# Kernel tuning notes

Hardware: AMD Instinct MI355X
Metric: run time of the kernel (lower is better)

## Reference

```python
import jax, jax.numpy as jnp
import numpy as np
from jax import lax

B, T, U, V = 4, 200, 100, 1024
D_ENC, D_DEC, J = 144, 320, 320


def setup_inputs() -> dict:
    key = jax.random.key(0)
    ks = jax.random.split(key, 8)
    s = lambda d: 1.0 / np.sqrt(d).astype(np.float32)
    return {
        "enc_out": jax.random.normal(ks[0], (B, T, D_ENC), jnp.float32),
        "dec_out": jax.random.normal(ks[1], (B, U + 1, D_DEC), jnp.float32),
        "W_enc": jax.random.normal(ks[2], (D_ENC, J), jnp.float32) * s(D_ENC),
        "b_enc": jnp.zeros((J,), jnp.float32),
        "W_dec": jax.random.normal(ks[3], (D_DEC, J), jnp.float32) * s(D_DEC),
        "b_dec": jnp.zeros((J,), jnp.float32),
        "W_out": jax.random.normal(ks[4], (J, V), jnp.float32) * s(J),
        "b_out": jnp.zeros((V,), jnp.float32),
        "targets": jax.random.randint(ks[5], (B, U), 1, V, jnp.int32),
        "enc_lengths": jax.random.randint(ks[6], (B,), T // 2, T + 1, jnp.int32),
        "target_lengths": jax.random.randint(ks[7], (B,), U // 2, U + 1, jnp.int32),
    }


def _rnnt_loss(log_probs, targets, enc_lengths, target_lengths):
    # log_probs: [B, T, U+1, V]; blank index = 0 (matches RNNTLoss(blank=0))
    blank_lp = log_probs[..., 0]  # [B, T, U+1]
    idx = jnp.broadcast_to(targets[:, None, :, None].astype(jnp.int32), (B, T, U, 1))
    emit_lp = jnp.take_along_axis(log_probs[:, :, :U, :], idx, axis=-1)[..., 0]  # [B, T, U]

    # alpha[0, u] = sum of emit log-probs along u at t=0
    alpha0 = jnp.concatenate(
        [jnp.zeros((B, 1), log_probs.dtype), jnp.cumsum(emit_lp[:, 0, :], axis=1)], axis=1
    )  # [B, U+1]

    def row(a, emit_t):
        # a: alpha_prev + blank (vertical transitions), [B, U+1]; emit_t: [B, U]
        def step(prev, xs):
            a_u, e_prev = xs
            cur = jnp.logaddexp(a_u, prev + e_prev)
            return cur, cur
        _, rest = lax.scan(step, a[:, 0], (a[:, 1:].T, emit_t.T))  # rest: [U, B]
        return jnp.concatenate([a[:, :1], rest.T], axis=1)

    def t_step(alpha_prev, xs):
        blank_prev, emit_t = xs
        alpha_t = row(alpha_prev + blank_prev, emit_t)
        return alpha_t, alpha_t

    xs = (jnp.swapaxes(blank_lp[:, :-1, :], 0, 1), jnp.swapaxes(emit_lp[:, 1:, :], 0, 1))
    _, alphas_rest = lax.scan(t_step, alpha0, xs)  # [T-1, B, U+1]
    alphas = jnp.concatenate([alpha0[None], alphas_rest], axis=0)  # [T, B, U+1]

    b_idx = jnp.arange(B)
    t_idx = enc_lengths - 1
    ll = alphas[t_idx, b_idx, target_lengths] + blank_lp[b_idx, t_idx, target_lengths]
    return jnp.mean(-ll)  # reduction='mean' over batch


def reference(enc_out, dec_out, W_enc, b_enc, W_dec, b_dec, W_out, b_out, targets, enc_lengths, target_lengths):
    enc_p = enc_out @ W_enc + b_enc  # [B, T, J]
    dec_p = dec_out @ W_dec + b_dec  # [B, U+1, J]
    joint = jnp.tanh(enc_p[:, :, None, :] + dec_p[:, None, :, :])  # [B, T, U+1, J]
    logits = joint @ W_out + b_out  # [B, T, U+1, V]
    log_probs = jax.nn.log_softmax(logits, axis=-1)
    return _rnnt_loss(log_probs, targets, enc_lengths, target_lengths)
```

## Files before the change

kernel.cpp:

```cpp
#include <hip/hip_runtime.h>
#include <math.h>

#define B_ 4
#define T_ 200
#define U_ 100
#define V_ 1024
#define DE 144
#define DD 320
#define J_ 320
#define M_TOT (B_ * T_ * (U_ + 1))
#define SSTR 328
#define DSTR 104
#define NDIAG 300

typedef __attribute__((ext_vector_type(8))) short bf16x8_t;
typedef __attribute__((ext_vector_type(4))) float f32x4_t;

__device__ __forceinline__ float fast_tanh(float x) {
    float e = __expf(2.0f * x);
    return 1.0f - __fdividef(2.0f, e + 1.0f);
}

__device__ __forceinline__ ushort f2bf(float x) {
    uint u = __float_as_uint(x);
    uint r = (u + 0x7FFFu + ((u >> 16) & 1u)) >> 16;
    return (ushort)r;
}

template <int K>
__global__ __launch_bounds__(J_) void proj_kernel(const float* __restrict__ X,
                                                  const float* __restrict__ W,
                                                  const float* __restrict__ bias,
                                                  float* __restrict__ Y) {
    __shared__ float sx[K];
    const int r = blockIdx.x;
    const int c = threadIdx.x;
    for (int k = threadIdx.x; k < K; k += J_) sx[k] = X[r * K + k];
    __syncthreads();
    float acc = bias[c];
#pragma unroll 4
    for (int k = 0; k < K; k++) acc = fmaf(sx[k], W[k * J_ + c], acc);
    Y[r * J_ + c] = acc;
}

__global__ __launch_bounds__(256) void wconv_kernel(const float* __restrict__ W,
                                                    ushort* __restrict__ Wt) {
    int idx = blockIdx.x * 256 + threadIdx.x;
    int k = idx >> 10;
    int v = idx & 1023;
    ushort b = f2bf(W[idx]);
    int frag = (v >> 4) * 10 + (k >> 5);
    int lane = (v & 15) | (((k >> 3) & 3) << 4);
    int elem = k & 7;
    Wt[frag * 512 + lane * 8 + elem] = b;
}

__global__ __launch_bounds__(1024, 4) void joint_mfma(
    const float* __restrict__ enc_p, const float* __restrict__ dec_p,
    const ushort* __restrict__ Wt, const float* __restrict__ b_out,
    const int* __restrict__ targets,
    float* __restrict__ bsk, float* __restrict__ esk) {
    __shared__ ushort sh[64 * SSTR];
    __shared__ float partm[16][64];
    __shared__ float parts[16][64];
    __shared__ float lse_sh[64];
    __shared__ int tgt_sh[64];

    const int tid = threadIdx.x;
    const int r0 = blockIdx.x * 64;

    for (int q = tid; q < 64 * 80; q += 1024) {
        int i = q / 80;
        int kq = q - i * 80;
        int k0 = kq * 4;
        int rc = r0 + i;
        if (rc > M_TOT - 1) rc = M_TOT - 1;
        int b = rc / 20200;
        int rem = rc - b * 20200;
        int t = rem / 101;
        int u = rem - t * 101;
        float4 e = *(const float4*)&enc_p[(b * 200 + t) * 320 + k0];
        float4 dd = *(const float4*)&dec_p[(b * 101 + u) * 320 + k0];
        ushort4 pk;
        pk.x = f2bf(fast_tanh(e.x + dd.x));
        pk.y = f2bf(fast_tanh(e.y + dd.y));
        pk.z = f2bf(fast_tanh(e.z + dd.z));
        pk.w = f2bf(fast_tanh(e.w + dd.w));
        *(ushort4*)&sh[i * SSTR + k0] = pk;
    }
    if (tid < 64) {
        int rc = r0 + tid;
        int tg = -1;
        if (rc < M_TOT) {
            int b = rc / 20200;
            int rem = rc - b * 20200;
            int u = rem - (rem / 101) * 101;
            if (u < U_) tg = targets[b * U_ + u];
        }
        tgt_sh[tid] = tg;
    }
    __syncthreads();

    const int wave = tid >> 6;
    const int lane = tid & 63;
    const int lrow = lane & 15;
    const int lk = (lane >> 4) * 8;
    const int cb16 = wave * 4;

    f32x4_t acc[4][4];
#pragma unroll
    for (int mt = 0; mt < 4; mt++)
#pragma unroll
        for (int nt = 0; nt < 4; nt++) acc[mt][nt] = (f32x4_t)(0.0f);

    for (int ks = 0; ks < 10; ks++) {
        bf16x8_t a[4];
#pragma unroll
        for (int mt = 0; mt < 4; mt++)
            a[mt] = *(const bf16x8_t*)&sh[(mt * 16 + lrow) * SSTR + ks * 32 + lk];
#pragma unroll
        for (int nt = 0; nt < 4; nt++) {
            bf16x8_t bfr = *(const bf16x8_t*)&Wt[(((cb16 + nt) * 10 + ks) << 9) + lane * 8];
#pragma unroll
            for (int mt = 0; mt < 4; mt++)
                acc[mt][nt] = __builtin_amdgcn_mfma_f32_16x16x32_bf16(a[mt], bfr, acc[mt][nt], 0, 0, 0);
        }
    }

    float bo[4];
#pragma unroll
    for (int nt = 0; nt < 4; nt++) bo[nt] = b_out[wave * 64 + nt * 16 + lrow];
#pragma unroll
    for (int mt = 0; mt < 4; mt++)
#pragma unroll
        for (int nt = 0; nt < 4; nt++) {
            acc[mt][nt].x += bo[nt];
            acc[mt][nt].y += bo[nt];
            acc[mt][nt].z += bo[nt];
            acc[mt][nt].w += bo[nt];
        }

#pragma unroll
    for (int mt = 0; mt < 4; mt++) {
#pragma unroll
        for (int j = 0; j < 4; j++) {
            float m = acc[mt][0][j];
#pragma unroll
            for (int nt = 1; nt < 4; nt++) m = fmaxf(m, acc[mt][nt][j]);
            float s = 0.0f;
#pragma unroll
            for (int nt = 0; nt < 4; nt++) s += __expf(acc[mt][nt][j] - m);
#pragma unroll
            for (int off = 1; off < 16; off <<= 1) {
                float mo = __shfl_xor(m, off, 16);
                float so = __shfl_xor(s, off, 16);
                float M = fmaxf(m, mo);
                s = s * __expf(m - M) + so * __expf(mo - M);
                m = M;
            }
            if (lrow == 0) {
                int row = mt * 16 + (lane >> 4) * 4 + j;
                partm[wave][row] = m;
                parts[wave][row] = s;
            }
        }
    }
    __syncthreads();
    if (tid < 64) {
        float m = partm[0][tid];
        float s = parts[0][tid];
#pragma unroll
        for (int w = 1; w < 16; w++) {
            float mo = partm[w][tid], so = parts[w][tid];
            float M = fmaxf(m, mo);
            s = s * __expf(m - M) + so * __expf(mo - M);
            m = M;
        }
        lse_sh[tid] = m + __logf(s);
    }
    __syncthreads();

#pragma unroll
    for (int mt = 0; mt < 4; mt++) {
#pragma unroll
        for (int j = 0; j < 4; j++) {
            int lr = mt * 16 + (lane >> 4) * 4 + j;
            int r = r0 + lr;
            if (r >= M_TOT) continue;
            int tc = tgt_sh[lr];
            bool isblank = (wave == 0) && (lrow == 0);
            bool isemit = (tc >= 0) && ((tc >> 6) == wave) && ((tc & 15) == lrow);
            if (isblank || isemit) {
                int b = r / 20200;
                int rem = r - b * 20200;
                int t = rem / 101;
                int u = rem - t * 101;
                float lse = lse_sh[lr];
                if (isblank)
                    bsk[(b * NDIAG + t + u) * DSTR + u] = acc[mt][0][j] - lse;
                if (isemit) {
                    int ntl = (tc >> 4) & 3;
                    float v = acc[mt][0][j];
#pragma unroll
                    for (int nt = 1; nt < 4; nt++)
                        if (nt == ntl) v = acc[mt][nt][j];
                    esk[(b * NDIAG + t + u) * DSTR + u] = v - lse;
                }
            }
        }
    }
}

__global__ __launch_bounds__(256) void alpha3_kernel(
    const float* __restrict__ bsk, const float* __restrict__ esk,
    const int* __restrict__ enc_len, const int* __restrict__ tgt_len,
    float* __restrict__ out) {
    __shared__ float ll_sh[B_];
    const int tid = threadIdx.x;
    const int b = tid >> 6;
    const int l = tid & 63;
    const float* Bp = bsk + b * (NDIAG * DSTR);
    const float* Ep = esk + b * (NDIAG * DSTR);
    const int el = enc_len[b];
    const int tl = tgt_len[b];
    const int dfin = el - 1 + tl;

    float a1 = (l == 0) ? 0.0f : -INFINITY;
    float a2 = -INFINITY;

    float c_b1 = Bp[l], c_b2 = Bp[64 + l];
    float c_e1 = Ep[l], c_e2 = Ep[64 + l];
    float m_b1 = Bp[DSTR + l], m_b2 = Bp[DSTR + 64 + l];
    float m_e1 = Ep[DSTR + l], m_e2 = Ep[DSTR + 64 + l];

    for (int d = 1; d <= NDIAG - 1; d++) {
        const int dn = (d + 1 <= NDIAG - 1) ? d + 1 : NDIAG - 1;
        float n_b1 = Bp[dn * DSTR + l], n_b2 = Bp[dn * DSTR + 64 + l];
        float n_e1 = Ep[dn * DSTR + l], n_e2 = Ep[dn * DSTR + 64 + l];

        float ce1 = __shfl_up(c_e1, 1, 64);
        float e1hi = __shfl(c_e1, 63, 64);
        float ce2s = __shfl_up(c_e2, 1, 64);
        float ce2 = (l == 0) ? e1hi : ce2s;
        float pa1 = __shfl_up(a1, 1, 64);
        float a1hi = __shfl(a1, 63, 64);
        float pa2s = __shfl_up(a2, 1, 64);
        float pa2 = (l == 0) ? a1hi : pa2s;

        const int t1 = d - l;
        float va = a1 + c_b1;
        float vb = (l >= 1) ? pa1 + ce1 : -INFINITY;
        float M = fmaxf(va, vb);
        float v1 = (M == -INFINITY) ? -INFINITY
                                    : M + __logf(1.0f + __expf(fminf(va, vb) - M));
        if (t1 < 0 || t1 >= T_ || l > U_) v1 = -INFINITY;

        const int t2 = d - 64 - l;
        float va2 = a2 + c_b2;
        float vb2 = pa2 + ce2;
        float M2 = fmaxf(va2, vb2);
        float v2 = (M2 == -INFINITY) ? -INFINITY
                                     : M2 + __logf(1.0f + __expf(fminf(va2, vb2) - M2));
        if (t2 < 0 || t2 >= T_ || (64 + l) > U_) v2 = -INFINITY;

        if (d == dfin) {
            if (l == tl) ll_sh[b] = v1 + m_b1;
            if (64 + l == tl) ll_sh[b] = v2 + m_b2;
        }

        a1 = v1; a2 = v2;
        c_b1 = m_b1; c_b2 = m_b2; c_e1 = m_e1; c_e2 = m_e2;
        m_b1 = n_b1; m_b2 = n_b2; m_e1 = n_e1; m_e2 = n_e2;
    }
    __syncthreads();
    if (tid == 0)
        out[0] = -0.25f * (ll_sh[0] + ll_sh[1] + ll_sh[2] + ll_sh[3]);
}

extern "C" void kernel_launch(void* const* d_in, const int* in_sizes, int n_in,
                              void* d_out, int out_size, void* d_ws, size_t ws_size,
                              hipStream_t stream) {
    const float* enc_out = (const float*)d_in[0];
    const float* dec_out = (const float*)d_in[1];
    const float* W_enc = (const float*)d_in[2];
    const float* b_enc = (const float*)d_in[3];
    const float* W_dec = (const float*)d_in[4];
    const float* b_dec = (const float*)d_in[5];
    const float* W_out = (const float*)d_in[6];
    const float* b_out = (const float*)d_in[7];
    const int* targets = (const int*)d_in[8];
    const int* enc_len = (const int*)d_in[9];
    const int* tgt_len = (const int*)d_in[10];

    float* ws = (float*)d_ws;
    float* enc_p = ws;
    float* dec_p = enc_p + B_ * T_ * J_;
    float* bsk = dec_p + B_ * (U_ + 1) * J_;
    float* esk = bsk + B_ * NDIAG * DSTR;
    ushort* Wt = (ushort*)(esk + B_ * NDIAG * DSTR);

    proj_kernel<DE><<<B_ * T_, J_, 0, stream>>>(enc_out, W_enc, b_enc, enc_p);
    proj_kernel<DD><<<B_ * (U_ + 1), J_, 0, stream>>>(dec_out, W_dec, b_dec, dec_p);
    wconv_kernel<<<(J_ * V_) / 256, 256, 0, stream>>>(W_out, Wt);

    joint_mfma<<<(M_TOT + 63) / 64, 1024, 0, stream>>>(
        enc_p, dec_p, Wt, b_out, targets, bsk, esk);

    alpha3_kernel<<<1, 256, 0, stream>>>(bsk, esk, enc_len, tgt_len, (float*)d_out);
}
```

Measured before the change: 237.0 us.

## Merge prep kernels, simplify softmax reduction, deepen alpha prefetch ring

Merges the two projection kernels and the W_out bf16 conversion into one launch, which removes two kernel launches and their serialization. In the joint kernel, the tanh staging loop is restructured so each thread handles one row with fixed addressing, and bf16 packing uses built-in paired conversion. The softmax reduction now finds the row max first and then sums exp2, replacing the online max/sum merge and its per-shuffle exps. The alpha recursion uses a 4-deep register ring so loads are issued further ahead of use, with the risk of indexing the register arrays dynamically.

```diff
diff --git a/kernel.cpp b/kernel.cpp
--- a/kernel.cpp
+++ b/kernel.cpp
@@ -1,4 +1,5 @@
 #include <hip/hip_runtime.h>
+#include <hip/hip_bf16.h>
 #include <math.h>
 
 #define B_ 4
@@ -12,13 +13,15 @@
 #define SSTR 328
 #define DSTR 104
 #define NDIAG 300
+#define LOG2E 1.4426950408889634f
 
 typedef __attribute__((ext_vector_type(8))) short bf16x8_t;
 typedef __attribute__((ext_vector_type(4))) float f32x4_t;
 
 __device__ __forceinline__ float fast_tanh(float x) {
-    float e = __expf(2.0f * x);
-    return 1.0f - __fdividef(2.0f, e + 1.0f);
+    float e = exp2f(x * (2.0f * LOG2E));
+    float r = __frcp_rn(e + 1.0f);
+    return fmaf(-2.0f, r, 1.0f);
 }
 
 __device__ __forceinline__ ushort f2bf(float x) {
@@ -27,32 +30,37 @@
     return (ushort)r;
 }
 
-template <int K>
-__global__ __launch_bounds__(J_) void proj_kernel(const float* __restrict__ X,
-                                                  const float* __restrict__ W,
-                                                  const float* __restrict__ bias,
-                                                  float* __restrict__ Y) {
-    __shared__ float sx[K];
-    const int r = blockIdx.x;
-    const int c = threadIdx.x;
-    for (int k = threadIdx.x; k < K; k += J_) sx[k] = X[r * K + k];
-    __syncthreads();
-    float acc = bias[c];
+__global__ __launch_bounds__(320) void prep_kernel(
+    const float* __restrict__ enc_out, const float* __restrict__ dec_out,
+    const float* __restrict__ W_enc, const float* __restrict__ b_enc,
+    const float* __restrict__ W_dec, const float* __restrict__ b_dec,
+    const float* __restrict__ W_out,
+    float* __restrict__ enc_p, float* __restrict__ dec_p,
+    ushort* __restrict__ Wt) {
+    const int bid = blockIdx.x;
+    const int tid = threadIdx.x;
+    if (bid < 1204) {
+        __shared__ float sx[320];
+        const float* X; const float* W; const float* bias; float* Y;
+        int K, r;
+        if (bid < 800) { X = enc_out; W = W_enc; bias = b_enc; Y = enc_p; K = DE; r = bid; }
+        else           { X = dec_out; W = W_dec; bias = b_dec; Y = dec_p; K = DD; r = bid - 800; }
+        for (int k = tid; k < K; k += 320) sx[k] = X[r * K + k];
+        __syncthreads();
+        float acc = bias[tid];
 #pragma unroll 4
-    for (int k = 0; k < K; k++) acc = fmaf(sx[k], W[k * J_ + c], acc);
-    Y[r * J_ + c] = acc;
-}
-
-__global__ __launch_bounds__(256) void wconv_kernel(const float* __restrict__ W,
-                                                    ushort* __restrict__ Wt) {
-    int idx = blockIdx.x * 256 + threadIdx.x;
-    int k = idx >> 10;
-    int v = idx & 1023;
-    ushort b = f2bf(W[idx]);
-    int frag = (v >> 4) * 10 + (k >> 5);
-    int lane = (v & 15) | (((k >> 3) & 3) << 4);
-    int elem = k & 7;
-    Wt[frag * 512 + lane * 8 + elem] = b;
+        for (int k = 0; k < K; k++) acc = fmaf(sx[k], W[k * J_ + tid], acc);
+        Y[r * J_ + tid] = acc;
+    } else {
+        int idx = (bid - 1204) * 320 + tid;
+        int k = idx >> 10;
+        int v = idx & 1023;
+        ushort b = f2bf(W_out[idx]);
+        int frag = (v >> 4) * 10 + (k >> 5);
+        int lane = (v & 15) | (((k >> 3) & 3) << 4);
+        int elem = k & 7;
+        Wt[frag * 512 + lane * 8 + elem] = b;
+    }
 }
 
 __global__ __launch_bounds__(1024, 4) void joint_mfma(
@@ -69,24 +77,34 @@
     const int tid = threadIdx.x;
     const int r0 = blockIdx.x * 64;
 
-    for (int q = tid; q < 64 * 80; q += 1024) {
-        int i = q / 80;
-        int kq = q - i * 80;
-        int k0 = kq * 4;
-        int rc = r0 + i;
+    {
+        const int si = tid >> 4;
+        const int sq = tid & 15;
+        int rc = r0 + si;
         if (rc > M_TOT - 1) rc = M_TOT - 1;
         int b = rc / 20200;
         int rem = rc - b * 20200;
         int t = rem / 101;
         int u = rem - t * 101;
-        float4 e = *(const float4*)&enc_p[(b * 200 + t) * 320 + k0];
-        float4 dd = *(const float4*)&dec_p[(b * 101 + u) * 320 + k0];
-        ushort4 pk;
-        pk.x = f2bf(fast_tanh(e.x + dd.x));
-        pk.y = f2bf(fast_tanh(e.y + dd.y));
-        pk.z = f2bf(fast_tanh(e.z + dd.z));
-        pk.w = f2bf(fast_tanh(e.w + dd.w));
-        *(ushort4*)&sh[i * SSTR + k0] = pk;
+        const float4* ep = (const float4*)&enc_p[(b * 200 + t) * 320];
+        const float4* dp = (const float4*)&dec_p[(b * 101 + u) * 320];
+        ushort* shp = &sh[si * SSTR];
+#pragma unroll
+        for (int it = 0; it < 5; it++) {
+            int kq = sq + it * 16;
+            float4 e = ep[kq];
+            float4 dd = dp[kq];
+            float t0 = fast_tanh(e.x + dd.x);
+            float t1 = fast_tanh(e.y + dd.y);
+            float t2 = fast_tanh(e.z + dd.z);
+            float t3 = fast_tanh(e.w + dd.w);
+            __hip_bfloat162 p0 = __float22bfloat162_rn(make_float2(t0, t1));
+            __hip_bfloat162 p1 = __float22bfloat162_rn(make_float2(t2, t3));
+            uint2 pk;
+            pk.x = *(uint*)&p0;
+            pk.y = *(uint*)&p1;
+            *(uint2*)&shp[kq * 4] = pk;
+        }
     }
     if (tid < 64) {
         int rc = r0 + tid;
@@ -133,31 +151,25 @@
 #pragma unroll
     for (int mt = 0; mt < 4; mt++)
 #pragma unroll
-        for (int nt = 0; nt < 4; nt++) {
-            acc[mt][nt].x += bo[nt];
-            acc[mt][nt].y += bo[nt];
-            acc[mt][nt].z += bo[nt];
-            acc[mt][nt].w += bo[nt];
-        }
+        for (int nt = 0; nt < 4; nt++) acc[mt][nt] += bo[nt];
 
 #pragma unroll
     for (int mt = 0; mt < 4; mt++) {
 #pragma unroll
         for (int j = 0; j < 4; j++) {
-            float m = acc[mt][0][j];
-#pragma unroll
-            for (int nt = 1; nt < 4; nt++) m = fmaxf(m, acc[mt][nt][j]);
-            float s = 0.0f;
-#pragma unroll
-            for (int nt = 0; nt < 4; nt++) s += __expf(acc[mt][nt][j] - m);
-#pragma unroll
-            for (int off = 1; off < 16; off <<= 1) {
-                float mo = __shfl_xor(m, off, 16);
-                float so = __shfl_xor(s, off, 16);
-                float M = fmaxf(m, mo);
-                s = s * __expf(m - M) + so * __expf(mo - M);
-                m = M;
-            }
+            float m = fmaxf(fmaxf(acc[mt][0][j], acc[mt][1][j]),
+                            fmaxf(acc[mt][2][j], acc[mt][3][j]));
+#pragma unroll
+            for (int off = 1; off < 16; off <<= 1)
+                m = fmaxf(m, __shfl_xor(m, off, 16));
+            float mm = m * LOG2E;
+            float s = exp2f(fmaf(acc[mt][0][j], LOG2E, -mm));
+            s += exp2f(fmaf(acc[mt][1][j], LOG2E, -mm));
+            s += exp2f(fmaf(acc[mt][2][j], LOG2E, -mm));
+            s += exp2f(fmaf(acc[mt][3][j], LOG2E, -mm));
+#pragma unroll
+            for (int off = 1; off < 16; off <<= 1)
+                s += __shfl_xor(s, off, 16);
             if (lrow == 0) {
                 int row = mt * 16 + (lane >> 4) * 4 + j;
                 partm[wave][row] = m;
@@ -211,7 +223,7 @@
     }
 }
 
-__global__ __launch_bounds__(256) void alpha3_kernel(
+__global__ __launch_bounds__(256) void alpha4_kernel(
     const float* __restrict__ bsk, const float* __restrict__ esk,
     const int* __restrict__ enc_len, const int* __restrict__ tgt_len,
     float* __restrict__ out) {
@@ -228,49 +240,65 @@
     float a1 = (l == 0) ? 0.0f : -INFINITY;
     float a2 = -INFINITY;
 
-    float c_b1 = Bp[l], c_b2 = Bp[64 + l];
-    float c_e1 = Ep[l], c_e2 = Ep[64 + l];
-    float m_b1 = Bp[DSTR + l], m_b2 = Bp[DSTR + 64 + l];
-    float m_e1 = Ep[DSTR + l], m_e2 = Ep[DSTR + 64 + l];
-
-    for (int d = 1; d <= NDIAG - 1; d++) {
-        const int dn = (d + 1 <= NDIAG - 1) ? d + 1 : NDIAG - 1;
-        float n_b1 = Bp[dn * DSTR + l], n_b2 = Bp[dn * DSTR + 64 + l];
-        float n_e1 = Ep[dn * DSTR + l], n_e2 = Ep[dn * DSTR + 64 + l];
-
-        float ce1 = __shfl_up(c_e1, 1, 64);
-        float e1hi = __shfl(c_e1, 63, 64);
-        float ce2s = __shfl_up(c_e2, 1, 64);
-        float ce2 = (l == 0) ? e1hi : ce2s;
-        float pa1 = __shfl_up(a1, 1, 64);
-        float a1hi = __shfl(a1, 63, 64);
-        float pa2s = __shfl_up(a2, 1, 64);
-        float pa2 = (l == 0) ? a1hi : pa2s;
-
-        const int t1 = d - l;
-        float va = a1 + c_b1;
-        float vb = (l >= 1) ? pa1 + ce1 : -INFINITY;
-        float M = fmaxf(va, vb);
-        float v1 = (M == -INFINITY) ? -INFINITY
-                                    : M + __logf(1.0f + __expf(fminf(va, vb) - M));
-        if (t1 < 0 || t1 >= T_ || l > U_) v1 = -INFINITY;
-
-        const int t2 = d - 64 - l;
-        float va2 = a2 + c_b2;
-        float vb2 = pa2 + ce2;
-        float M2 = fmaxf(va2, vb2);
-        float v2 = (M2 == -INFINITY) ? -INFINITY
-                                     : M2 + __logf(1.0f + __expf(fminf(va2, vb2) - M2));
-        if (t2 < 0 || t2 >= T_ || (64 + l) > U_) v2 = -INFINITY;
-
-        if (d == dfin) {
-            if (l == tl) ll_sh[b] = v1 + m_b1;
-            if (64 + l == tl) ll_sh[b] = v2 + m_b2;
-        }
-
-        a1 = v1; a2 = v2;
-        c_b1 = m_b1; c_b2 = m_b2; c_e1 = m_e1; c_e2 = m_e2;
-        m_b1 = n_b1; m_b2 = n_b2; m_e1 = n_e1; m_e2 = n_e2;
+    float rb1[4], rb2[4], re1[4], re2[4];
+#pragma unroll
+    for (int k = 0; k < 4; k++) {
+        rb1[k] = Bp[k * DSTR + l];
+        rb2[k] = Bp[k * DSTR + 64 + l];
+        re1[k] = Ep[k * DSTR + l];
+        re2[k] = Ep[k * DSTR + 64 + l];
+    }
+
+    for (int dc = 1; dc <= 297; dc += 4) {
+#pragma unroll
+        for (int q = 0; q < 4; q++) {
+            const int d = dc + q;
+            if (d > NDIAG - 1) continue;
+            const int sc = (d - 1) & 3;
+            const int sm = d & 3;
+            float cb1 = rb1[sc], cb2 = rb2[sc], ce1 = re1[sc], ce2 = re2[sc];
+            float mb1 = rb1[sm], mb2 = rb2[sm];
+            int dn = d + 3;
+            if (dn > NDIAG - 1) dn = NDIAG - 1;
+            rb1[sc] = Bp[dn * DSTR + l];
+            rb2[sc] = Bp[dn * DSTR + 64 + l];
+            re1[sc] = Ep[dn * DSTR + l];
+            re2[sc] = Ep[dn * DSTR + 64 + l];
+
+            float pe1 = __shfl_up(ce1, 1, 64);
+            float e1hi = __shfl(ce1, 63, 64);
+            float pe2s = __shfl_up(ce2, 1, 64);
+            float pe2 = (l == 0) ? e1hi : pe2s;
+            float pa1 = __shfl_up(a1, 1, 64);
+            float a1hi = __shfl(a1, 63, 64);
+            float pa2s = __shfl_up(a2, 1, 64);
+            float pa2 = (l == 0) ? a1hi : pa2s;
+
+            const int t1 = d - l;
+            float va = a1 + cb1;
+            float vb = (l >= 1) ? pa1 + pe1 : -INFINITY;
+            float M = fmaxf(va, vb);
+            float v1 = (M == -INFINITY)
+                           ? -INFINITY
+                           : M + __logf(1.0f + __expf(fminf(va, vb) - M));
+            if (t1 < 0 || t1 >= T_ || l > U_) v1 = -INFINITY;
+
+            const int t2 = d - 64 - l;
+            float va2 = a2 + cb2;
+            float vb2 = pa2 + pe2;
+            float M2 = fmaxf(va2, vb2);
+            float v2 = (M2 == -INFINITY)
+                           ? -INFINITY
+                           : M2 + __logf(1.0f + __expf(fminf(va2, vb2) - M2));
+            if (t2 < 0 || t2 >= T_ || (64 + l) > U_) v2 = -INFINITY;
+
+            if (d == dfin) {
+                if (l == tl) ll_sh[b] = v1 + mb1;
+                if (64 + l == tl) ll_sh[b] = v2 + mb2;
+            }
+            a1 = v1;
+            a2 = v2;
+        }
     }
     __syncthreads();
     if (tid == 0)
@@ -299,12 +327,11 @@
     float* esk = bsk + B_ * NDIAG * DSTR;
     ushort* Wt = (ushort*)(esk + B_ * NDIAG * DSTR);
 
-    proj_kernel<DE><<<B_ * T_, J_, 0, stream>>>(enc_out, W_enc, b_enc, enc_p);
-    proj_kernel<DD><<<B_ * (U_ + 1), J_, 0, stream>>>(dec_out, W_dec, b_dec, dec_p);
-    wconv_kernel<<<(J_ * V_) / 256, 256, 0, stream>>>(W_out, Wt);
+    prep_kernel<<<2228, 320, 0, stream>>>(enc_out, dec_out, W_enc, b_enc,
+                                          W_dec, b_dec, W_out, enc_p, dec_p, Wt);
 
     joint_mfma<<<(M_TOT + 63) / 64, 1024, 0, stream>>>(
         enc_p, dec_p, Wt, b_out, targets, bsk, esk);
 
-    alpha3_kernel<<<1, 256, 0, stream>>>(bsk, esk, enc_len, tgt_len, (float*)d_out);
-}
+    alpha4_kernel<<<1, 256, 0, stream>>>(bsk, esk, enc_len, tgt_len, (float*)d_out);
+}
```

Result: faster. 218.0 us (-8.0%).
